# Kernel tuning notes

Hardware: AMD Instinct MI355X
Metric: run time of the kernel (lower is better)

The kernel has to match this reference:

```python
import jax, jax.numpy as jnp
import numpy as np

SAMPLE_RATE = 16000
SOUND_SPEED = 343.0
MAX_ORDER = 15
RIR_LENGTH = 3968
WINDOW_LENGTH = 81
PAD = WINDOW_LENGTH // 2  # 40

# Static image-source lattice (depends only on max_order): all integer
# reflection index triplets with |nx|+|ny|+|nz| <= max_order.
_ind = np.arange(-MAX_ORDER, MAX_ORDER + 1)
_grid = np.stack(np.meshgrid(_ind, _ind, _ind, indexing="ij"), -1).reshape(-1, 3)
XYZ = _grid[np.abs(_grid).sum(1) <= MAX_ORDER].astype(np.float32)  # (I,3), I=4991
EXP_LO = np.abs(np.floor(XYZ / 2)).astype(np.float32)        # hits on lower walls per dim
EXP_HI = np.abs(np.floor((XYZ + 1) / 2)).astype(np.float32)  # hits on upper walls per dim


def _hann(x, T):
    # continuous Hann window sampled at non-integer points, zero outside |x|<=T/2
    return jnp.where(jnp.abs(x) <= T / 2, 0.5 * (1.0 + jnp.cos(2.0 * jnp.pi * x / T)), 0.0)


def _forward(inp):
    room = inp[:, 0:3]                 # (B,3) room dimensions [m]
    mic = inp[:, 3:6] * room           # (B,3)
    src = inp[:, 6:9] * room           # (B,3)
    a_w = inp[:, 9:10]
    absorption = jnp.concatenate([a_w, a_w, a_w, a_w, inp[:, 10:11], inp[:, 11:12]], axis=1)
    absorption = absorption * 0.84 + 0.01            # (B,6): [x-,x+,y-,y+,floor,ceiling]
    tr = jnp.sqrt(1.0 - absorption)                  # wall reflection coefficients

    xyz = jnp.asarray(XYZ)                           # (I,3)
    d = room[:, None, :]
    s = src[:, None, :]
    # image source locations (B,I,3): mirror parity per torchaudio ISM
    img_loc = jnp.where(xyz % 2 == 1, d * (xyz + 1.0) - s, d * xyz + s)
    # per-image-source attenuation (B,I)
    t_lo = tr[:, None, 0::2]                         # (B,1,3) lower walls per dim
    t_hi = tr[:, None, 1::2]                         # (B,1,3) upper walls per dim
    att = jnp.prod(t_lo ** jnp.asarray(EXP_LO) * t_hi ** jnp.asarray(EXP_HI), axis=-1)

    dist = jnp.linalg.norm(img_loc - mic[:, None, :], axis=-1)   # (B,I)
    amp = att / dist                                              # 1/r spreading
    delay = dist * (SAMPLE_RATE / SOUND_SPEED)                    # fractional sample delay
    delay_i = jnp.ceil(delay)

    # windowed-sinc fractional-delay pulse sampled at n = delay_i-PAD .. delay_i+PAD
    n_rel = jnp.arange(-PAD, PAD + 1, dtype=jnp.float32)          # (W,)
    x = delay_i[..., None] + n_rel - delay[..., None]             # (B,I,W)
    sig = amp[..., None] * jnp.sinc(x) * _hann(x, 2 * PAD)        # (B,I,W)

    # scatter-accumulate pulses at time index n, dropping out-of-range samples
    t_idx = (delay_i[..., None] + n_rel).astype(jnp.int32)        # (B,I,W)
    B = inp.shape[0]
    b_idx = jnp.arange(B, dtype=jnp.int32)[:, None, None]
    rir = jnp.zeros((B, RIR_LENGTH), dtype=sig.dtype).at[b_idx, t_idx].add(sig, mode="drop")

    toa = PAD + SAMPLE_RATE * jnp.linalg.norm(mic - src, axis=1) / SOUND_SPEED  # (B,)
    return rir, toa


def setup_inputs():
    key = jax.random.key(0)
    u = jax.random.uniform(key, (128, 12), dtype=jnp.float32)
    room = 2.0 + 8.0 * u[:, :3]          # room dims in [2,10] m
    rest = 0.05 + 0.9 * u[:, 3:]         # mic/src fractions and absorptions in (0,1)
    return {"input": jnp.concatenate([room, rest], axis=1)}


def reference(input):
    return _forward(input)
```

## Files before the change

### kernel.cpp

```cpp
#include <hip/hip_runtime.h>

#define NIMG    4991
#define RIRLEN  3968
#define NT      512
#define NGRP    4
#define INV_PI  0.31830988618379067f
#define SR_OVER_C 46.647230320699704f

struct Tab { int v[NIMG]; };
static constexpr Tab make_tab() {
    Tab t{};
    int k = 0;
    for (int x = -15; x <= 15; ++x)
        for (int y = -15; y <= 15; ++y)
            for (int z = -15; z <= 15; ++z) {
                int ax = x < 0 ? -x : x;
                int ay = y < 0 ? -y : y;
                int az = z < 0 ? -z : z;
                if (ax + ay + az <= 15)
                    t.v[k++] = (x + 15) | ((y + 15) << 8) | ((z + 15) << 16);
            }
    return t;
}
__constant__ Tab c_tab = make_tab();

static __device__ __forceinline__ int iabs(int v) { return v < 0 ? -v : v; }

typedef __fp16 f16x2 __attribute__((ext_vector_type(2)));

__global__ __launch_bounds__(NT)
void rir_fused(const float* __restrict__ inp, float* __restrict__ out, int B) {
    const int bx   = blockIdx.x;
    const int b    = bx >> 2;
    const int g    = bx & 3;
    const int tid  = threadIdx.x;
    const int lane = tid & 63;
    const int wv   = tid >> 6;
    const int q    = lane & 3;

    __shared__ float2   s_dh[NIMG];
    __shared__ unsigned s_cs[NIMG];
    __shared__ float    s_par[12];
    __shared__ int      s_h4[4][256];
    __shared__ int      s_off[257];

    for (int k = tid; k < 1024; k += NT) ((int*)s_h4)[k] = 0;
    if (tid == 0) {
        const float* ip = inp + b * 12;
        float rx = ip[0], ry = ip[1], rz = ip[2];
        float mx = ip[3] * rx, my = ip[4] * ry, mz = ip[5] * rz;
        float sx = ip[6] * rx, sy = ip[7] * ry, sz = ip[8] * rz;
        float aw = __builtin_fmaf(ip[9],  0.84f, 0.01f);
        float a4 = __builtin_fmaf(ip[10], 0.84f, 0.01f);
        float a5 = __builtin_fmaf(ip[11], 0.84f, 0.01f);
        s_par[0] = rx; s_par[1] = ry; s_par[2] = rz;
        s_par[3] = mx; s_par[4] = my; s_par[5] = mz;
        s_par[6] = sx; s_par[7] = sy; s_par[8] = sz;
        s_par[9]  = 0.5f * __builtin_amdgcn_logf(1.0f - aw);
        s_par[10] = 0.5f * __builtin_amdgcn_logf(1.0f - a4);
        s_par[11] = 0.5f * __builtin_amdgcn_logf(1.0f - a5);
        if (g == 0) {
            float dx = mx - sx, dy = my - sy, dz = mz - sz;
            out[(size_t)B * RIRLEN + b] = __builtin_fmaf(
                __builtin_sqrtf(dx * dx + dy * dy + dz * dz), SR_OVER_C, 40.0f);
        }
    }
    __syncthreads();

    const float rx = s_par[0], ry = s_par[1], rz = s_par[2];
    const float mx = s_par[3], my = s_par[4], mz = s_par[5];
    const float sx = s_par[6], sy = s_par[7], sz = s_par[8];
    const float lw = s_par[9], l4 = s_par[10], l5 = s_par[11];

    for (int idx = tid; idx < NIMG; idx += NT) {
        const int p = c_tab.v[idx];
        const int x = (p & 255) - 15;
        const int y = ((p >> 8) & 255) - 15;
        const int z = ((p >> 16) & 255) - 15;
        const float ix = (x & 1) ? __builtin_fmaf(rx, (float)(x + 1), -sx)
                                 : __builtin_fmaf(rx, (float)x, sx);
        const float iy = (y & 1) ? __builtin_fmaf(ry, (float)(y + 1), -sy)
                                 : __builtin_fmaf(ry, (float)y, sy);
        const float iz = (z & 1) ? __builtin_fmaf(rz, (float)(z + 1), -sz)
                                 : __builtin_fmaf(rz, (float)z, sz);
        const float dx = ix - mx, dy = iy - my, dz = iz - mz;
        const float dist  = __builtin_sqrtf(__builtin_fmaf(dx, dx, __builtin_fmaf(dy, dy, dz * dz)));
        const float delay = dist * SR_OVER_C;
        const int   ti0   = (int)__builtin_ceilf(delay) - 40;
        if (ti0 < RIRLEN) atomicAdd(&s_h4[q][(ti0 + 96) >> 4], 1);
    }
    __syncthreads();

    if (tid < 256)
        s_off[tid + 1] = s_h4[0][tid] + s_h4[1][tid] + s_h4[2][tid] + s_h4[3][tid];
    if (tid == 0) s_off[0] = 0;
    __syncthreads();
    for (int d = 1; d < 256; d <<= 1) {
        int tv = 0;
        if (tid < 256 && tid >= d) tv = s_off[tid + 1 - d];
        __syncthreads();
        if (tid < 256 && tid >= d) s_off[tid + 1] += tv;
        __syncthreads();
    }
    if (tid < 256) {
        int run = s_off[tid];
        #pragma unroll
        for (int p = 0; p < 4; ++p) {
            const int c = s_h4[p][tid];
            s_h4[p][tid] = run;
            run += c;
        }
    }
    __syncthreads();

    for (int idx = tid; idx < NIMG; idx += NT) {
        const int p = c_tab.v[idx];
        const int x = (p & 255) - 15;
        const int y = ((p >> 8) & 255) - 15;
        const int z = ((p >> 16) & 255) - 15;
        const float ix = (x & 1) ? __builtin_fmaf(rx, (float)(x + 1), -sx)
                                 : __builtin_fmaf(rx, (float)x, sx);
        const float iy = (y & 1) ? __builtin_fmaf(ry, (float)(y + 1), -sy)
                                 : __builtin_fmaf(ry, (float)y, sy);
        const float iz = (z & 1) ? __builtin_fmaf(rz, (float)(z + 1), -sz)
                                 : __builtin_fmaf(rz, (float)z, sz);
        const float dx = ix - mx, dy = iy - my, dz = iz - mz;
        const float dist  = __builtin_sqrtf(__builtin_fmaf(dx, dx, __builtin_fmaf(dy, dy, dz * dz)));
        const float delay = dist * SR_OVER_C;
        const float di    = __builtin_ceilf(delay);
        const int   ti0   = (int)di - 40;
        if (ti0 >= RIRLEN) continue;

        const int ew = iabs(x >> 1) + iabs((x + 1) >> 1) + iabs(y >> 1) + iabs((y + 1) >> 1);
        const float att = __builtin_amdgcn_exp2f(__builtin_fmaf((float)ew, lw,
                              __builtin_fmaf((float)iabs(z >> 1), l4,
                                   (float)iabs((z + 1) >> 1) * l5)));
        const float amp = att * __builtin_amdgcn_rcpf(dist);
        float frac = di - delay;
        if (frac == 0.0f) frac = di * 1.52587890625e-05f;
        const int dii = (int)di;
        float c1p = amp * __builtin_amdgcn_sinf(0.5f * frac) * INV_PI;
        if (dii & 1) c1p = -c1p;
        const float dstore = di - frac;

        const float rv = dstore * 0.0125f;
        const float fr = rv - __builtin_floorf(rv);
        const float cd = __builtin_amdgcn_cosf(fr);
        const float sd = __builtin_amdgcn_sinf(fr);
        const f16x2 pk2 = __builtin_amdgcn_cvt_pkrtz(cd, sd);

        const int slot = atomicAdd(&s_h4[q][(ti0 + 96) >> 4], 1);
        s_dh[slot] = make_float2(dstore, 0.5f * c1p);
        s_cs[slot] = __builtin_bit_cast(unsigned, pk2);
    }
    __syncthreads();

    #pragma unroll
    for (int ws = 0; ws < 2; ++ws) {
        const int wi = g + 4 * wv + 32 * ws;
        if (wi >= 62) break;
        const int lo = s_off[4 * wi + 1];
        const int hi = s_off[4 * wi + 10];

        const int   t    = (wi << 6) + lane;
        const float tf   = (float)t;
        const int   m    = t - (t / 80) * 80;
        const float cth0 = __builtin_amdgcn_cosf((float)m * 0.0125f);
        const float sth0 = __builtin_amdgcn_sinf((float)m * 0.0125f);
        const float sl   = (lane & 1) ? -1.0f : 1.0f;

        float acc = 0.0f;
        #pragma unroll 4
        for (int i = lo; i < hi; ++i) {
            const float2   e  = s_dh[i];
            const unsigned pk = s_cs[i];
            const f16x2    h  = __builtin_bit_cast(f16x2, pk);
            const float xw = tf - e.x;
            const float u  = __builtin_fmaf(cth0, (float)h.x,
                                 __builtin_fmaf(sth0, (float)h.y, 1.0f));
            const float hm = (__builtin_fabsf(xw) <= 40.0f) ? (e.y * u) : 0.0f;
            float v = hm * __builtin_amdgcn_rcpf(xw);
            v = (xw == 0.0f) ? 0.0f : v;
            acc += v;
        }
        out[(size_t)b * RIRLEN + t] = sl * acc;
    }
}

extern "C" void kernel_launch(void* const* d_in, const int* in_sizes, int n_in,
                              void* d_out, int out_size, void* d_ws, size_t ws_size,
                              hipStream_t stream) {
    (void)d_ws; (void)ws_size; (void)n_in; (void)out_size;
    const float* inp = (const float*)d_in[0];
    float* out = (float*)d_out;
    const int B = in_sizes[0] / 12;
    rir_fused<<<dim3(B * NGRP), dim3(NT), 0, stream>>>(inp, out, B);
}
```

Before: 111.3 us.

## Cache image-source data in registers, halve blocks per batch, balance windows across waves

Each thread now does the full per-image computation once, keeps the results in registers, and writes them to their sorted slot after the prefix scan. The second recomputation pass is gone. Blocks per batch item drop from four to two, and each block's 31 output windows go to waves in proportion to their workload. The inner loop folds amplitude into the f16 cos/sin terms so each entry needs one FMA chain, at the cost of some f16 precision and more register pressure. The histogram layout is also transposed.

After: 105.2 us. 5.5% less time.

```diff
diff --git a/kernel.cpp b/kernel.cpp
--- a/kernel.cpp
+++ b/kernel.cpp
@@ -3,7 +3,8 @@
 #define NIMG    4991
 #define RIRLEN  3968
 #define NT      512
-#define NGRP    4
+#define NW      31
+#define KPT     10
 #define INV_PI  0.31830988618379067f
 #define SR_OVER_C 46.647230320699704f
 
@@ -31,8 +32,8 @@
 __global__ __launch_bounds__(NT)
 void rir_fused(const float* __restrict__ inp, float* __restrict__ out, int B) {
     const int bx   = blockIdx.x;
-    const int b    = bx >> 2;
-    const int g    = bx & 3;
+    const int b    = bx >> 1;
+    const int g    = bx & 1;
     const int tid  = threadIdx.x;
     const int lane = tid & 63;
     const int wv   = tid >> 6;
@@ -41,7 +42,7 @@
     __shared__ float2   s_dh[NIMG];
     __shared__ unsigned s_cs[NIMG];
     __shared__ float    s_par[12];
-    __shared__ int      s_h4[4][256];
+    __shared__ int      s_h4[256][4];
     __shared__ int      s_off[257];
 
     for (int k = tid; k < 1024; k += NT) ((int*)s_h4)[k] = 0;
@@ -72,27 +73,62 @@
     const float sx = s_par[6], sy = s_par[7], sz = s_par[8];
     const float lw = s_par[9], l4 = s_par[10], l5 = s_par[11];
 
-    for (int idx = tid; idx < NIMG; idx += NT) {
-        const int p = c_tab.v[idx];
-        const int x = (p & 255) - 15;
-        const int y = ((p >> 8) & 255) - 15;
-        const int z = ((p >> 16) & 255) - 15;
-        const float ix = (x & 1) ? __builtin_fmaf(rx, (float)(x + 1), -sx)
-                                 : __builtin_fmaf(rx, (float)x, sx);
-        const float iy = (y & 1) ? __builtin_fmaf(ry, (float)(y + 1), -sy)
-                                 : __builtin_fmaf(ry, (float)y, sy);
-        const float iz = (z & 1) ? __builtin_fmaf(rz, (float)(z + 1), -sz)
-                                 : __builtin_fmaf(rz, (float)z, sz);
-        const float dx = ix - mx, dy = iy - my, dz = iz - mz;
-        const float dist  = __builtin_sqrtf(__builtin_fmaf(dx, dx, __builtin_fmaf(dy, dy, dz * dz)));
-        const float delay = dist * SR_OVER_C;
-        const int   ti0   = (int)__builtin_ceilf(delay) - 40;
-        if (ti0 < RIRLEN) atomicAdd(&s_h4[q][(ti0 + 96) >> 4], 1);
+    float2   edh[KPT];
+    unsigned ecs[KPT];
+    int      bkt[KPT];
+    #pragma unroll
+    for (int k = 0; k < KPT; ++k) {
+        bkt[k] = -1;
+        const int idx = tid + k * NT;
+        if (idx < NIMG) {
+            const int p = c_tab.v[idx];
+            const int x = (p & 255) - 15;
+            const int y = ((p >> 8) & 255) - 15;
+            const int z = ((p >> 16) & 255) - 15;
+            const float ix = (x & 1) ? __builtin_fmaf(rx, (float)(x + 1), -sx)
+                                     : __builtin_fmaf(rx, (float)x, sx);
+            const float iy = (y & 1) ? __builtin_fmaf(ry, (float)(y + 1), -sy)
+                                     : __builtin_fmaf(ry, (float)y, sy);
+            const float iz = (z & 1) ? __builtin_fmaf(rz, (float)(z + 1), -sz)
+                                     : __builtin_fmaf(rz, (float)z, sz);
+            const float dx = ix - mx, dy = iy - my, dz = iz - mz;
+            const float dist  = __builtin_sqrtf(
+                __builtin_fmaf(dx, dx, __builtin_fmaf(dy, dy, dz * dz)));
+            const float delay = dist * SR_OVER_C;
+            const float di    = __builtin_ceilf(delay);
+            const int   ti0   = (int)di - 40;
+            if (ti0 < RIRLEN) {
+                const int ew = iabs(x >> 1) + iabs((x + 1) >> 1)
+                             + iabs(y >> 1) + iabs((y + 1) >> 1);
+                const float att = __builtin_amdgcn_exp2f(__builtin_fmaf((float)ew, lw,
+                                      __builtin_fmaf((float)iabs(z >> 1), l4,
+                                           (float)iabs((z + 1) >> 1) * l5)));
+                const float amp = att * __builtin_amdgcn_rcpf(dist);
+                float frac = di - delay;
+                if (frac == 0.0f) frac = di * 1.52587890625e-05f;
+                const int dii = (int)di;
+                float c1p = amp * __builtin_amdgcn_sinf(0.5f * frac) * INV_PI;
+                if (dii & 1) c1p = -c1p;
+                const float Hp     = 0.5f * c1p;
+                const float dstore = di - frac;
+                const float rv = dstore * 0.0125f;
+                const float fr = rv - __builtin_floorf(rv);
+                const float Hcd = Hp * __builtin_amdgcn_cosf(fr);
+                const float Hsd = Hp * __builtin_amdgcn_sinf(fr);
+                const f16x2 pk2 = __builtin_amdgcn_cvt_pkrtz(Hcd, Hsd);
+
+                const int bk = (ti0 + 96) >> 4;
+                bkt[k] = bk;
+                edh[k] = make_float2(dstore, Hp);
+                ecs[k] = __builtin_bit_cast(unsigned, pk2);
+                atomicAdd(&s_h4[bk][q], 1);
+            }
+        }
     }
     __syncthreads();
 
     if (tid < 256)
-        s_off[tid + 1] = s_h4[0][tid] + s_h4[1][tid] + s_h4[2][tid] + s_h4[3][tid];
+        s_off[tid + 1] = s_h4[tid][0] + s_h4[tid][1] + s_h4[tid][2] + s_h4[tid][3];
     if (tid == 0) s_off[0] = 0;
     __syncthreads();
     for (int d = 1; d < 256; d <<= 1) {
@@ -106,61 +142,42 @@
         int run = s_off[tid];
         #pragma unroll
         for (int p = 0; p < 4; ++p) {
-            const int c = s_h4[p][tid];
-            s_h4[p][tid] = run;
+            const int c = s_h4[tid][p];
+            s_h4[tid][p] = run;
             run += c;
         }
     }
     __syncthreads();
 
-    for (int idx = tid; idx < NIMG; idx += NT) {
-        const int p = c_tab.v[idx];
-        const int x = (p & 255) - 15;
-        const int y = ((p >> 8) & 255) - 15;
-        const int z = ((p >> 16) & 255) - 15;
-        const float ix = (x & 1) ? __builtin_fmaf(rx, (float)(x + 1), -sx)
-                                 : __builtin_fmaf(rx, (float)x, sx);
-        const float iy = (y & 1) ? __builtin_fmaf(ry, (float)(y + 1), -sy)
-                                 : __builtin_fmaf(ry, (float)y, sy);
-        const float iz = (z & 1) ? __builtin_fmaf(rz, (float)(z + 1), -sz)
-                                 : __builtin_fmaf(rz, (float)z, sz);
-        const float dx = ix - mx, dy = iy - my, dz = iz - mz;
-        const float dist  = __builtin_sqrtf(__builtin_fmaf(dx, dx, __builtin_fmaf(dy, dy, dz * dz)));
-        const float delay = dist * SR_OVER_C;
-        const float di    = __builtin_ceilf(delay);
-        const int   ti0   = (int)di - 40;
-        if (ti0 >= RIRLEN) continue;
-
-        const int ew = iabs(x >> 1) + iabs((x + 1) >> 1) + iabs(y >> 1) + iabs((y + 1) >> 1);
-        const float att = __builtin_amdgcn_exp2f(__builtin_fmaf((float)ew, lw,
-                              __builtin_fmaf((float)iabs(z >> 1), l4,
-                                   (float)iabs((z + 1) >> 1) * l5)));
-        const float amp = att * __builtin_amdgcn_rcpf(dist);
-        float frac = di - delay;
-        if (frac == 0.0f) frac = di * 1.52587890625e-05f;
-        const int dii = (int)di;
-        float c1p = amp * __builtin_amdgcn_sinf(0.5f * frac) * INV_PI;
-        if (dii & 1) c1p = -c1p;
-        const float dstore = di - frac;
-
-        const float rv = dstore * 0.0125f;
-        const float fr = rv - __builtin_floorf(rv);
-        const float cd = __builtin_amdgcn_cosf(fr);
-        const float sd = __builtin_amdgcn_sinf(fr);
-        const f16x2 pk2 = __builtin_amdgcn_cvt_pkrtz(cd, sd);
-
-        const int slot = atomicAdd(&s_h4[q][(ti0 + 96) >> 4], 1);
-        s_dh[slot] = make_float2(dstore, 0.5f * c1p);
-        s_cs[slot] = __builtin_bit_cast(unsigned, pk2);
-    }
-    __syncthreads();
-
     #pragma unroll
-    for (int ws = 0; ws < 2; ++ws) {
-        const int wi = g + 4 * wv + 32 * ws;
-        if (wi >= 62) break;
-        const int lo = s_off[4 * wi + 1];
-        const int hi = s_off[4 * wi + 10];
+    for (int k = 0; k < KPT; ++k) {
+        if (bkt[k] >= 0) {
+            const int slot = atomicAdd(&s_h4[bkt[k]][q], 1);
+            s_dh[slot] = edh[k];
+            s_cs[slot] = ecs[k];
+        }
+    }
+    __syncthreads();
+
+    int T = 0;
+    #pragma unroll
+    for (int kk = 0; kk < NW; ++kk) {
+        const int wi = g + 2 * kk;
+        T += s_off[4 * wi + 10] - s_off[4 * wi + 1];
+    }
+
+    int P = 0;
+    for (int kk = 0; kk < NW; ++kk) {
+        const int wi  = g + 2 * kk;
+        const int lo  = s_off[4 * wi + 1];
+        const int hi  = s_off[4 * wi + 10];
+        const int len = hi - lo;
+        int owner = (T > 0)
+            ? (int)((8u * (unsigned)(P + (len >> 1))) / (unsigned)T)
+            : (kk >> 2);
+        if (owner > 7) owner = 7;
+        P += len;
+        if (owner != wv) continue;
 
         const int   t    = (wi << 6) + lane;
         const float tf   = (float)t;
@@ -172,16 +189,13 @@
         float acc = 0.0f;
         #pragma unroll 4
         for (int i = lo; i < hi; ++i) {
-            const float2   e  = s_dh[i];
-            const unsigned pk = s_cs[i];
-            const f16x2    h  = __builtin_bit_cast(f16x2, pk);
-            const float xw = tf - e.x;
-            const float u  = __builtin_fmaf(cth0, (float)h.x,
-                                 __builtin_fmaf(sth0, (float)h.y, 1.0f));
-            const float hm = (__builtin_fabsf(xw) <= 40.0f) ? (e.y * u) : 0.0f;
-            float v = hm * __builtin_amdgcn_rcpf(xw);
-            v = (xw == 0.0f) ? 0.0f : v;
-            acc += v;
+            const float2 e  = s_dh[i];
+            const f16x2  h  = __builtin_bit_cast(f16x2, s_cs[i]);
+            const float xw  = tf - e.x;
+            const float pre = __builtin_fmaf(cth0, (float)h.x,
+                                  __builtin_fmaf(sth0, (float)h.y, e.y));
+            const float hm  = (__builtin_fabsf(xw) <= 40.0f) ? pre : 0.0f;
+            acc = __builtin_fmaf(hm, __builtin_amdgcn_rcpf(xw), acc);
         }
         out[(size_t)b * RIRLEN + t] = sl * acc;
     }
@@ -194,5 +208,5 @@
     const float* inp = (const float*)d_in[0];
     float* out = (float*)d_out;
     const int B = in_sizes[0] / 12;
-    rir_fused<<<dim3(B * NGRP), dim3(NT), 0, stream>>>(inp, out, B);
+    rir_fused<<<dim3(B * 2), dim3(NT), 0, stream>>>(inp, out, B);
 }
```
